# Performance work log

Measured on AMD Instinct MI355X. Metric: run time of the kernel, lower is better.

The kernel has to match this reference:

```python
import jax, jax.numpy as jnp
import numpy as np

N_NODES = 100000
N_EDGES = 3200000
N_GRAPHS = 512
IN_DIM = 128
H1, H2 = 32, 64
OUT_DIM = 1
LN_EPS = 1e-5


def setup_inputs() -> dict:
    key = jax.random.key(0)
    ks = jax.random.split(key, 12)
    x = jax.random.normal(ks[0], (N_NODES, IN_DIM), dtype=jnp.float32)
    edge_index = jax.random.randint(ks[1], (2, N_EDGES), 0, N_NODES, dtype=jnp.int64)
    batch = jnp.sort(jax.random.randint(ks[2], (N_NODES,), 0, N_GRAPHS, dtype=jnp.int64))
    def lin(k, fi, fo):
        s = 1.0 / np.sqrt(fi)
        return jax.random.uniform(k, (fi, fo), minval=-s, maxval=s, dtype=jnp.float32)
    params = {
        'W1': lin(ks[3], IN_DIM, H1), 'b1': jnp.zeros((H1,), jnp.float32),
        'g1': jnp.ones((H1,), jnp.float32), 'be1': jnp.zeros((H1,), jnp.float32),
        'W2': lin(ks[4], H1, H2), 'b2': jnp.zeros((H2,), jnp.float32),
        'g2': jnp.ones((H2,), jnp.float32), 'be2': jnp.zeros((H2,), jnp.float32),
        'Wc1': lin(ks[5], H2, 32), 'bc1': jnp.zeros((32,), jnp.float32),
        'Wc2': lin(ks[6], 32, OUT_DIM), 'bc2': jnp.zeros((OUT_DIM,), jnp.float32),
    }
    return {'x': x, 'edge_index': edge_index, 'batch': batch, **params}


def _gcn_norm(edge_index, n):
    # add self loops (PyG GCNConv default)
    loop = jnp.arange(n, dtype=edge_index.dtype)
    src = jnp.concatenate([edge_index[0], loop])
    dst = jnp.concatenate([edge_index[1], loop])
    deg = jax.ops.segment_sum(jnp.ones_like(dst, dtype=jnp.float32), dst, num_segments=n)
    dinv = jnp.where(deg > 0, 1.0 / jnp.sqrt(deg), 0.0)
    norm = dinv[src] * dinv[dst]  # [E+N]
    return src, dst, norm


def _gcn_conv(x, src, dst, norm, W, b, n):
    h = x @ W                                    # tiny GEMM
    msg = h[src] * norm[:, None]                 # gather + scale (memory-bound)
    agg = jax.ops.segment_sum(msg, dst, num_segments=n)  # scatter-add
    return agg + b


def _layernorm(x, g, b):
    mu = jnp.mean(x, axis=-1, keepdims=True)
    var = jnp.mean(jnp.square(x - mu), axis=-1, keepdims=True)
    return (x - mu) * jax.lax.rsqrt(var + LN_EPS) * g + b


def reference(x, edge_index, batch, W1, b1, g1, be1, W2, b2, g2, be2, Wc1, bc1, Wc2, bc2):
    n = x.shape[0]
    src, dst, norm = _gcn_norm(edge_index, n)
    # layer 1: GCNConv -> LayerNorm -> ReLU (dropout = identity in eval)
    h = jax.nn.relu(_layernorm(_gcn_conv(x, src, dst, norm, W1, b1, n), g1, be1))
    # layer 2
    h = jax.nn.relu(_layernorm(_gcn_conv(h, src, dst, norm, W2, b2, n), g2, be2))
    # global mean pool over graphs
    sums = jax.ops.segment_sum(h, batch, num_segments=N_GRAPHS)
    cnts = jax.ops.segment_sum(jnp.ones((n,), h.dtype), batch, num_segments=N_GRAPHS)
    pooled = sums / jnp.maximum(cnts, 1.0)[:, None]  # [G, H2]
    # classifier MLP
    z = jax.nn.relu(pooled @ Wc1 + bc1)
    return z @ Wc2 + bc2
```

## Files before the change

### kernel.cpp

```cpp
#include <hip/hip_runtime.h>
#include <hip/hip_fp16.h>

#define CAP 10240

__global__ __launch_bounds__(1024) void k_fused1(const int* __restrict__ ei,
                                                 const float* __restrict__ x,
                                                 const float* __restrict__ W1,
                                                 const int* __restrict__ batch,
                                                 int* __restrict__ gcnt,
                                                 int* __restrict__ bucketed,
                                                 __half* __restrict__ hs,
                                                 int* __restrict__ gstart,
                                                 int nA, int nG1, int NB,
                                                 int n, int E, int G) {
    __shared__ __align__(16) char smem[40960];
    int tid = threadIdx.x;
    int bid = blockIdx.x;
    if (bid < nA) {
        int* hist = (int*)smem;
        int* excl = hist + 512;
        int* gb   = excl + 512;
        int* ebuf = gb + 512;
        const int* src = ei;
        const int* dst = ei + E;
        for (int i = tid; i < 512; i += 1024) hist[i] = 0;
        __syncthreads();
        int e0 = bid * 8192;
        int d[8], sR[8];
#pragma unroll
        for (int k = 0; k < 8; k++) {
            int e = e0 + k * 1024 + tid;
            bool v = e < E;
            d[k]  = v ? dst[e] : -1;
            sR[k] = v ? src[e] : 0;
            if (v) atomicAdd(&hist[d[k] >> 8], 1);
        }
        __syncthreads();
        if (tid < 512) excl[tid] = hist[tid];
        __syncthreads();
        for (int off = 1; off < 512; off <<= 1) {
            int v2 = 0;
            if (tid < 512) v2 = excl[tid] + ((tid >= off) ? excl[tid - off] : 0);
            __syncthreads();
            if (tid < 512) excl[tid] = v2;
            __syncthreads();
        }
        if (tid < 512) {
            int c = hist[tid];
            int ex = excl[tid] - c;
            excl[tid] = ex;
            gb[tid] = c ? atomicAdd(&gcnt[tid], c) : 0;
            hist[tid] = ex;
        }
        __syncthreads();
#pragma unroll
        for (int k = 0; k < 8; k++) {
            if (d[k] >= 0) {
                int b = d[k] >> 8;
                int p = atomicAdd(&hist[b], 1);
                ebuf[p] = (sR[k] << 8) | (d[k] & 255);
            }
        }
        __syncthreads();
        if (tid < 512) {
            int lds0 = excl[tid];
            int cnt  = hist[tid] - lds0;
            int gb0  = gb[tid];
            int* dstp = bucketed + (size_t)tid * CAP;
            for (int k = 0; k < cnt; k++) {
                int gp = gb0 + k;
                if (gp < CAP) dstp[gp] = ebuf[lds0 + k];
            }
        }
    } else if (bid < nA + nG1) {
        float* Ws = (float*)smem;
        const float4* W4 = (const float4*)W1;
        ((float4*)Ws)[tid] = W4[tid];
        __syncthreads();
        int gb2 = bid - nA;
        int row = gb2 * 128 + (tid >> 3);
        int g8 = tid & 7;
        if (row >= n) return;
        const float4* x4 = (const float4*)x;
        const float4* Ws4 = (const float4*)Ws;
        float a0 = 0.f, a1 = 0.f, a2 = 0.f, a3 = 0.f;
#pragma unroll 4
        for (int j = 0; j < 32; j++) {
            float4 xq = x4[(size_t)row * 32 + j];
#pragma unroll
            for (int t = 0; t < 4; t++) {
                float xv = (t == 0) ? xq.x : (t == 1) ? xq.y : (t == 2) ? xq.z : xq.w;
                float4 wv = Ws4[(4 * j + t) * 8 + g8];
                a0 += xv * wv.x; a1 += xv * wv.y; a2 += xv * wv.z; a3 += xv * wv.w;
            }
        }
        __half2 o[2] = { __floats2half2_rn(a0, a1), __floats2half2_rn(a2, a3) };
        *(float2*)(hs + (size_t)row * 32 + g8 * 4) = *(const float2*)o;
    } else {
        int i = (bid - nA - nG1) * 1024 + tid;
        if (i > n) return;
        if (i == 0) {
            for (int g = 0; g <= batch[0]; g++) gstart[g] = 0;
        } else if (i == n) {
            for (int g = batch[n - 1] + 1; g <= G; g++) gstart[g] = n;
        } else {
            int b = batch[i], p = batch[i - 1];
            for (int g = p + 1; g <= b; g++) gstart[g] = i;
        }
    }
}

__global__ __launch_bounds__(512) void k_bucketB(const int* __restrict__ bucketed,
                                                 const int* __restrict__ gcnt,
                                                 int* __restrict__ csr,
                                                 int* __restrict__ offs,
                                                 int* __restrict__ deg,
                                                 float* __restrict__ dinv,
                                                 __half* __restrict__ hs, int n) {
    __shared__ int hist[256], scan_a[256], scan_b[256];
    __shared__ float sdinv[256];
    int b = blockIdx.x;
    int tid = threadIdx.x;
    int cnt = min(gcnt[b], CAP);
    int base = b * CAP;
    const int* ent = bucketed + (size_t)b * CAP;
    if (tid < 256) hist[tid] = 0;
    __syncthreads();
    for (int i = tid; i < cnt; i += 512) atomicAdd(&hist[ent[i] & 255], 1);
    __syncthreads();
    int h = (tid < 256) ? hist[tid] : 0;
    if (tid < 256) scan_a[tid] = h;
    __syncthreads();
    int* cur = scan_a;
    int* nxt = scan_b;
    for (int off = 1; off < 256; off <<= 1) {
        if (tid < 256) nxt[tid] = cur[tid] + ((tid >= off) ? cur[tid - off] : 0);
        __syncthreads();
        int* tmp = cur; cur = nxt; nxt = tmp;
    }
    if (tid < 256) {
        int ex = cur[tid] - h;
        float dv = rsqrtf((float)(h + 1));
        sdinv[tid] = dv;
        int node = b * 256 + tid;
        if (node < n) {
            offs[node] = base + ex;
            deg[node] = h;
            dinv[node] = dv;
        }
        hist[tid] = ex;
    }
    __syncthreads();
    for (int i = tid; i < cnt; i += 512) {
        int v = ent[i];
        int p = atomicAdd(&hist[v & 255], 1);
        csr[base + p] = v >> 8;
    }
    float4* hsv = (float4*)hs;
#pragma unroll
    for (int p = 0; p < 2; p++) {
        int idx = p * 512 + tid;
        int nl = idx >> 2, cg = idx & 3;
        int node = b * 256 + nl;
        if (node < n) {
            float dv = sdinv[nl];
            float4 raw = hsv[(size_t)node * 4 + cg];
            __half2* h2 = (__half2*)&raw;
            __half2 o[4];
#pragma unroll
            for (int j = 0; j < 4; j++) {
                float2 f = __half22float2(h2[j]);
                o[j] = __floats2half2_rn(f.x * dv, f.y * dv);
            }
            hsv[(size_t)node * 4 + cg] = *(const float4*)o;
        }
    }
}

template <bool DO_LN>
__global__ __launch_bounds__(256) void k_gather(const __half* __restrict__ hs,
                                                const int* __restrict__ csr,
                                                const int* __restrict__ offs,
                                                const int* __restrict__ deg,
                                                const float* __restrict__ dinv,
                                                const float* __restrict__ b,
                                                const float* __restrict__ g,
                                                const float* __restrict__ be,
                                                __half* __restrict__ out, int n) {
    int wave = threadIdx.x >> 6;
    int lane = threadIdx.x & 63;
    int q   = lane >> 4;
    int l16 = lane & 15;
    int nb  = l16 >> 2;
    int cg  = l16 & 3;
    int row = blockIdx.x * 16 + wave * 4 + q;
    if (row >= n) return;
    int base = offs[row];
    int dg = deg[row];
    const float4* hsv = (const float4*)hs;
    const float4 fz = make_float4(0.f, 0.f, 0.f, 0.f);
    const __half2 hz = __floats2half2_rn(0.f, 0.f);
    __half2 ha0[4], ha1[4];
#pragma unroll
    for (int j = 0; j < 4; j++) { ha0[j] = hz; ha1[j] = hz; }

    int e = nb;
    float4 r0 = (e     < dg) ? hsv[(size_t)csr[base + e    ] * 4 + cg] : fz;
    float4 r1 = (e + 4 < dg) ? hsv[(size_t)csr[base + e + 4] * 4 + cg] : fz;
    while (e < dg) {
        float4 p0 = (e +  8 < dg) ? hsv[(size_t)csr[base + e +  8] * 4 + cg] : fz;
        float4 p1 = (e + 12 < dg) ? hsv[(size_t)csr[base + e + 12] * 4 + cg] : fz;
        const __half2* h0 = (const __half2*)&r0;
        const __half2* h1 = (const __half2*)&r1;
#pragma unroll
        for (int j = 0; j < 4; j++) {
            ha0[j] = __hadd2(ha0[j], h0[j]);
            ha1[j] = __hadd2(ha1[j], h1[j]);
        }
        r0 = p0; r1 = p1; e += 8;
    }
    float acc[8];
#pragma unroll
    for (int j = 0; j < 4; j++) {
        float2 f0 = __half22float2(ha0[j]);
        float2 f1 = __half22float2(ha1[j]);
        acc[2 * j]     = f0.x + f1.x;
        acc[2 * j + 1] = f0.y + f1.y;
    }
#pragma unroll
    for (int m = 4; m <= 8; m <<= 1)
#pragma unroll
        for (int j = 0; j < 8; j++) acc[j] += __shfl_xor(acc[j], m, 64);
    float dv = dinv[row];
    float4 sraw = hsv[(size_t)row * 4 + cg];
    const __half2* sh2 = (const __half2*)&sraw;
    float a[8];
#pragma unroll
    for (int j = 0; j < 4; j++) {
        float2 f = __half22float2(sh2[j]);
        a[2 * j]     = (acc[2 * j]     + f.x) * dv;
        a[2 * j + 1] = (acc[2 * j + 1] + f.y) * dv;
    }
    if (DO_LN) {
        int c0 = cg * 8;
        float s = 0.f;
#pragma unroll
        for (int j = 0; j < 8; j++) { a[j] += b[c0 + j]; s += a[j]; }
#pragma unroll
        for (int m = 1; m <= 2; m <<= 1) s += __shfl_xor(s, m, 64);
        float mu = s * (1.0f / 32.0f);
        float v2 = 0.f;
#pragma unroll
        for (int j = 0; j < 8; j++) { a[j] -= mu; v2 += a[j] * a[j]; }
#pragma unroll
        for (int m = 1; m <= 2; m <<= 1) v2 += __shfl_xor(v2, m, 64);
        float inv = rsqrtf(v2 * (1.0f / 32.0f) + 1e-5f);
#pragma unroll
        for (int j = 0; j < 8; j++)
            a[j] = fmaxf(a[j] * inv * g[c0 + j] + be[c0 + j], 0.f) * dv;
    }
    if (nb == 0) {
        __half2 o[4];
#pragma unroll
        for (int j = 0; j < 4; j++) o[j] = __floats2half2_rn(a[2 * j], a[2 * j + 1]);
        ((float4*)out)[(size_t)row * 4 + cg] = *(const float4*)o;
    }
}

__global__ __launch_bounds__(512) void k_pool_cls(const __half* __restrict__ agg2,
                                                  const float* __restrict__ W2,
                                                  const float* __restrict__ b2,
                                                  const float* __restrict__ g2,
                                                  const float* __restrict__ be2,
                                                  const int* __restrict__ gstart,
                                                  const float* __restrict__ Wc1,
                                                  const float* __restrict__ bc1,
                                                  const float* __restrict__ Wc2,
                                                  const float* __restrict__ bc2,
                                                  float* __restrict__ out) {
    __shared__ float Ws[32 * 64];
    __shared__ float red[8 * 64];
    int tid = threadIdx.x;
    for (int i = tid; i < 32 * 64; i += 512) Ws[i] = W2[i];
    int g = blockIdx.x;
    int r0 = gstart[g], r1 = gstart[g + 1];
    int wave = tid >> 6, lane = tid & 63;
    float pacc = 0.0f;
    __syncthreads();
    for (int row = r0 + wave; row < r1; row += 8) {
        const float4* a4 = (const float4*)(agg2 + (size_t)row * 32);
        float4 r4[4];
#pragma unroll
        for (int q = 0; q < 4; q++) r4[q] = a4[q];
        const __half2* ah = (const __half2*)r4;
        float acc = b2[lane];
#pragma unroll
        for (int k2 = 0; k2 < 16; k2++) {
            float2 f = __half22float2(ah[k2]);
            acc += f.x * Ws[(2 * k2) * 64 + lane] + f.y * Ws[(2 * k2 + 1) * 64 + lane];
        }
        float s = acc;
#pragma unroll
        for (int m = 32; m >= 1; m >>= 1) s += __shfl_xor(s, m, 64);
        float mu = s * (1.0f / 64.0f);
        float d = acc - mu;
        float v = d * d;
#pragma unroll
        for (int m = 32; m >= 1; m >>= 1) v += __shfl_xor(v, m, 64);
        float val = d * rsqrtf(v * (1.0f / 64.0f) + 1e-5f) * g2[lane] + be2[lane];
        pacc += fmaxf(val, 0.0f);
    }
    red[wave * 64 + lane] = pacc;
    __syncthreads();
    if (wave == 0) {
        float p = 0.f;
#pragma unroll
        for (int w = 0; w < 8; w++) p += red[w * 64 + lane];
        p *= 1.0f / fmaxf((float)(r1 - r0), 1.0f);
        red[lane] = p;
    }
    __syncthreads();
    if (wave == 0 && lane < 32) {
        float zs = bc1[lane];
#pragma unroll
        for (int k = 0; k < 64; k++) zs += red[k] * Wc1[k * 32 + lane];
        float o = fmaxf(zs, 0.0f) * Wc2[lane];
#pragma unroll
        for (int m = 16; m >= 1; m >>= 1) o += __shfl_xor(o, m, 64);
        if (lane == 0) out[g] = o + bc2[0];
    }
}


extern "C" void kernel_launch(void* const* d_in, const int* in_sizes, int n_in,
                              void* d_out, int out_size, void* d_ws, size_t ws_size,
                              hipStream_t stream) {
    const float* x     = (const float*)d_in[0];
    const int*   ei    = (const int*)d_in[1];
    const int*   batch = (const int*)d_in[2];
    const float* W1  = (const float*)d_in[3];
    const float* b1  = (const float*)d_in[4];
    const float* g1  = (const float*)d_in[5];
    const float* be1 = (const float*)d_in[6];
    const float* W2  = (const float*)d_in[7];
    const float* b2  = (const float*)d_in[8];
    const float* g2  = (const float*)d_in[9];
    const float* be2 = (const float*)d_in[10];
    const float* Wc1 = (const float*)d_in[11];
    const float* bc1 = (const float*)d_in[12];
    const float* Wc2 = (const float*)d_in[13];
    const float* bc2 = (const float*)d_in[14];

    int n = in_sizes[0] / 128;
    int E = in_sizes[1] / 2;
    int G = out_size;
    int NB = (n + 255) >> 8;

    float* ws     = (float*)d_ws;
    float* dinv   = ws;
    int*   deg    = (int*)(dinv + n);
    int*   offs   = deg + n;
    int*   gcnt   = offs + n;
    int*   gstart = gcnt + 512;
    int*   csr    = gstart + 516;
    __half* hsA   = (__half*)(csr + (size_t)NB * CAP);
    int*   bucketed = (int*)(hsA + (size_t)n * 32);
    __half* hsB   = (__half*)bucketed;

    int nA  = (E + 8191) / 8192;
    int nG1 = (n + 127) / 128;
    int nGs = (n + 1024) / 1024;

    hipMemsetAsync(gcnt, 0, 512 * sizeof(int), stream);

    k_fused1<<<nA + nG1 + nGs, 1024, 0, stream>>>(ei, x, W1, batch, gcnt, bucketed,
                                                  hsA, gstart, nA, nG1, NB, n, E, G);
    k_bucketB<<<NB, 512, 0, stream>>>(bucketed, gcnt, csr, offs, deg, dinv, hsA, n);

    k_gather<true><<<(n + 15) / 16, 256, 0, stream>>>(hsA, csr, offs, deg, dinv,
                                                      b1, g1, be1, hsB, n);
    k_gather<false><<<(n + 15) / 16, 256, 0, stream>>>(hsB, csr, offs, deg, dinv,
                                                       nullptr, nullptr, nullptr, hsA, n);
    k_pool_cls<<<G, 512, 0, stream>>>(hsA, W2, b2, g2, be2, gstart,
                                      Wc1, bc1, Wc2, bc2, (float*)d_out);
}
```

Baseline: 215.1 us.

## Split feature columns into halves so each gather pass fits in cache

Stores the 32-wide half-precision node features as two 16-column planes and runs the neighbor gather separately on each plane. The intent is that each 3.2 MB plane stays resident in L2/MALL during random gathers. LayerNorm moves into a separate kernel, the final dinv scaling of layer 2 is folded into the pooling kernel, and the bucket copy-out is spread over 16 lanes per bucket. The cost is two extra gather launches plus one LN launch, re-reading the CSR indices for each half, and half-width rows per gather, which use fewer bytes per index fetched.

```diff
diff --git a/kernel.cpp b/kernel.cpp
--- a/kernel.cpp
+++ b/kernel.cpp
@@ -9,7 +9,8 @@
                                                  const int* __restrict__ batch,
                                                  int* __restrict__ gcnt,
                                                  int* __restrict__ bucketed,
-                                                 __half* __restrict__ hs,
+                                                 __half* __restrict__ hLo,
+                                                 __half* __restrict__ hHi,
                                                  int* __restrict__ gstart,
                                                  int nA, int nG1, int NB,
                                                  int n, int E, int G) {
@@ -62,15 +63,14 @@
             }
         }
         __syncthreads();
-        if (tid < 512) {
-            int lds0 = excl[tid];
-            int cnt  = hist[tid] - lds0;
-            int gb0  = gb[tid];
-            int* dstp = bucketed + (size_t)tid * CAP;
-            for (int k = 0; k < cnt; k++) {
-                int gp = gb0 + k;
-                if (gp < CAP) dstp[gp] = ebuf[lds0 + k];
-            }
+        int grp = tid >> 4, l = tid & 15;
+        for (int t = grp; t < 512; t += 64) {
+            int lds0 = excl[t];
+            int cnt  = hist[t] - lds0;
+            int gb0  = gb[t];
+            int* dstp = bucketed + (size_t)t * CAP + gb0;
+            for (int k = l; k < cnt; k += 16)
+                if (gb0 + k < CAP) dstp[k] = ebuf[lds0 + k];
         }
     } else if (bid < nA + nG1) {
         float* Ws = (float*)smem;
@@ -95,7 +95,9 @@
             }
         }
         __half2 o[2] = { __floats2half2_rn(a0, a1), __floats2half2_rn(a2, a3) };
-        *(float2*)(hs + (size_t)row * 32 + g8 * 4) = *(const float2*)o;
+        __half* dstp = (g8 < 4) ? (hLo + (size_t)row * 16 + g8 * 4)
+                                : (hHi + (size_t)row * 16 + (g8 - 4) * 4);
+        *(float2*)dstp = *(const float2*)o;
     } else {
         int i = (bid - nA - nG1) * 1024 + tid;
         if (i > n) return;
@@ -116,7 +118,8 @@
                                                  int* __restrict__ offs,
                                                  int* __restrict__ deg,
                                                  float* __restrict__ dinv,
-                                                 __half* __restrict__ hs, int n) {
+                                                 __half* __restrict__ hLo,
+                                                 __half* __restrict__ hHi, int n) {
     __shared__ int hist[256], scan_a[256], scan_b[256];
     __shared__ float sdinv[256];
     int b = blockIdx.x;
@@ -156,7 +159,8 @@
         int p = atomicAdd(&hist[v & 255], 1);
         csr[base + p] = v >> 8;
     }
-    float4* hsv = (float4*)hs;
+    float4* lo = (float4*)hLo;
+    float4* hi = (float4*)hHi;
 #pragma unroll
     for (int p = 0; p < 2; p++) {
         int idx = p * 512 + tid;
@@ -164,7 +168,9 @@
         int node = b * 256 + nl;
         if (node < n) {
             float dv = sdinv[nl];
-            float4 raw = hsv[(size_t)node * 4 + cg];
+            float4* ptr = (cg < 2) ? &lo[(size_t)node * 2 + cg]
+                                   : &hi[(size_t)node * 2 + (cg - 2)];
+            float4 raw = *ptr;
             __half2* h2 = (__half2*)&raw;
             __half2 o[4];
 #pragma unroll
@@ -172,28 +178,23 @@
                 float2 f = __half22float2(h2[j]);
                 o[j] = __floats2half2_rn(f.x * dv, f.y * dv);
             }
-            hsv[(size_t)node * 4 + cg] = *(const float4*)o;
-        }
-    }
-}
-
-template <bool DO_LN>
-__global__ __launch_bounds__(256) void k_gather(const __half* __restrict__ hs,
-                                                const int* __restrict__ csr,
-                                                const int* __restrict__ offs,
-                                                const int* __restrict__ deg,
-                                                const float* __restrict__ dinv,
-                                                const float* __restrict__ b,
-                                                const float* __restrict__ g,
-                                                const float* __restrict__ be,
-                                                __half* __restrict__ out, int n) {
+            *ptr = *(const float4*)o;
+        }
+    }
+}
+
+__global__ __launch_bounds__(256) void k_gather_h(const __half* __restrict__ hs,
+                                                  const int* __restrict__ csr,
+                                                  const int* __restrict__ offs,
+                                                  const int* __restrict__ deg,
+                                                  __half* __restrict__ out, int n) {
     int wave = threadIdx.x >> 6;
     int lane = threadIdx.x & 63;
-    int q   = lane >> 4;
-    int l16 = lane & 15;
-    int nb  = l16 >> 2;
-    int cg  = l16 & 3;
-    int row = blockIdx.x * 16 + wave * 4 + q;
+    int o  = lane >> 3;
+    int l8 = lane & 7;
+    int nb = l8 >> 1;
+    int cg = l8 & 1;
+    int row = blockIdx.x * 32 + wave * 8 + o;
     if (row >= n) return;
     int base = offs[row];
     int dg = deg[row];
@@ -205,11 +206,11 @@
     for (int j = 0; j < 4; j++) { ha0[j] = hz; ha1[j] = hz; }
 
     int e = nb;
-    float4 r0 = (e     < dg) ? hsv[(size_t)csr[base + e    ] * 4 + cg] : fz;
-    float4 r1 = (e + 4 < dg) ? hsv[(size_t)csr[base + e + 4] * 4 + cg] : fz;
+    float4 r0 = (e     < dg) ? hsv[(size_t)csr[base + e    ] * 2 + cg] : fz;
+    float4 r1 = (e + 4 < dg) ? hsv[(size_t)csr[base + e + 4] * 2 + cg] : fz;
     while (e < dg) {
-        float4 p0 = (e +  8 < dg) ? hsv[(size_t)csr[base + e +  8] * 4 + cg] : fz;
-        float4 p1 = (e + 12 < dg) ? hsv[(size_t)csr[base + e + 12] * 4 + cg] : fz;
+        float4 p0 = (e +  8 < dg) ? hsv[(size_t)csr[base + e +  8] * 2 + cg] : fz;
+        float4 p1 = (e + 12 < dg) ? hsv[(size_t)csr[base + e + 12] * 2 + cg] : fz;
         const __half2* h0 = (const __half2*)&r0;
         const __half2* h1 = (const __half2*)&r1;
 #pragma unroll
@@ -228,46 +229,74 @@
         acc[2 * j + 1] = f0.y + f1.y;
     }
 #pragma unroll
-    for (int m = 4; m <= 8; m <<= 1)
+    for (int m = 2; m <= 4; m <<= 1)
 #pragma unroll
         for (int j = 0; j < 8; j++) acc[j] += __shfl_xor(acc[j], m, 64);
+    float4 sraw = hsv[(size_t)row * 2 + cg];
+    const __half2* sh2 = (const __half2*)&sraw;
+    if (nb == 0) {
+        __half2 ov[4];
+#pragma unroll
+        for (int j = 0; j < 4; j++) {
+            float2 f = __half22float2(sh2[j]);
+            ov[j] = __floats2half2_rn(acc[2 * j] + f.x, acc[2 * j + 1] + f.y);
+        }
+        ((float4*)out)[(size_t)row * 2 + cg] = *(const float4*)ov;
+    }
+}
+
+__global__ __launch_bounds__(256) void k_ln_split(const __half* __restrict__ aggLo,
+                                                  const __half* __restrict__ aggHi,
+                                                  const float* __restrict__ dinv,
+                                                  const float* __restrict__ b,
+                                                  const float* __restrict__ g,
+                                                  const float* __restrict__ be,
+                                                  __half* __restrict__ outLo,
+                                                  __half* __restrict__ outHi, int n) {
+    int tid = threadIdx.x;
+    int rl = tid >> 2;
+    int l4 = tid & 3;
+    int row = blockIdx.x * 64 + rl;
+    if (row >= n) return;
+    const float4* lo = (const float4*)aggLo;
+    const float4* hi = (const float4*)aggHi;
+    float4 raw = (l4 < 2) ? lo[(size_t)row * 2 + l4] : hi[(size_t)row * 2 + (l4 - 2)];
     float dv = dinv[row];
-    float4 sraw = hsv[(size_t)row * 4 + cg];
-    const __half2* sh2 = (const __half2*)&sraw;
+    int c0 = l4 * 8;
+    const __half2* h2 = (const __half2*)&raw;
     float a[8];
+    float s = 0.f;
 #pragma unroll
     for (int j = 0; j < 4; j++) {
-        float2 f = __half22float2(sh2[j]);
-        a[2 * j]     = (acc[2 * j]     + f.x) * dv;
-        a[2 * j + 1] = (acc[2 * j + 1] + f.y) * dv;
-    }
-    if (DO_LN) {
-        int c0 = cg * 8;
-        float s = 0.f;
-#pragma unroll
-        for (int j = 0; j < 8; j++) { a[j] += b[c0 + j]; s += a[j]; }
-#pragma unroll
-        for (int m = 1; m <= 2; m <<= 1) s += __shfl_xor(s, m, 64);
-        float mu = s * (1.0f / 32.0f);
-        float v2 = 0.f;
-#pragma unroll
-        for (int j = 0; j < 8; j++) { a[j] -= mu; v2 += a[j] * a[j]; }
-#pragma unroll
-        for (int m = 1; m <= 2; m <<= 1) v2 += __shfl_xor(v2, m, 64);
-        float inv = rsqrtf(v2 * (1.0f / 32.0f) + 1e-5f);
-#pragma unroll
-        for (int j = 0; j < 8; j++)
-            a[j] = fmaxf(a[j] * inv * g[c0 + j] + be[c0 + j], 0.f) * dv;
-    }
-    if (nb == 0) {
-        __half2 o[4];
-#pragma unroll
-        for (int j = 0; j < 4; j++) o[j] = __floats2half2_rn(a[2 * j], a[2 * j + 1]);
-        ((float4*)out)[(size_t)row * 4 + cg] = *(const float4*)o;
-    }
-}
-
-__global__ __launch_bounds__(512) void k_pool_cls(const __half* __restrict__ agg2,
+        float2 f = __half22float2(h2[j]);
+        a[2 * j]     = f.x * dv + b[c0 + 2 * j];
+        a[2 * j + 1] = f.y * dv + b[c0 + 2 * j + 1];
+        s += a[2 * j] + a[2 * j + 1];
+    }
+#pragma unroll
+    for (int m = 1; m <= 2; m <<= 1) s += __shfl_xor(s, m, 64);
+    float mu = s * (1.0f / 32.0f);
+    float v2 = 0.f;
+#pragma unroll
+    for (int j = 0; j < 8; j++) { a[j] -= mu; v2 += a[j] * a[j]; }
+#pragma unroll
+    for (int m = 1; m <= 2; m <<= 1) v2 += __shfl_xor(v2, m, 64);
+    float inv = rsqrtf(v2 * (1.0f / 32.0f) + 1e-5f);
+    __half2 ov[4];
+#pragma unroll
+    for (int j = 0; j < 4; j++) {
+        float y0 = fmaxf(a[2 * j]     * inv * g[c0 + 2 * j]     + be[c0 + 2 * j],     0.f) * dv;
+        float y1 = fmaxf(a[2 * j + 1] * inv * g[c0 + 2 * j + 1] + be[c0 + 2 * j + 1], 0.f) * dv;
+        ov[j] = __floats2half2_rn(y0, y1);
+    }
+    float4* dstp = (l4 < 2) ? ((float4*)outLo + (size_t)row * 2 + l4)
+                            : ((float4*)outHi + (size_t)row * 2 + (l4 - 2));
+    *dstp = *(const float4*)ov;
+}
+
+__global__ __launch_bounds__(512) void k_pool_cls(const __half* __restrict__ aggLo,
+                                                  const __half* __restrict__ aggHi,
+                                                  const float* __restrict__ dinv,
                                                   const float* __restrict__ W2,
                                                   const float* __restrict__ b2,
                                                   const float* __restrict__ g2,
@@ -287,18 +316,23 @@
     int wave = tid >> 6, lane = tid & 63;
     float pacc = 0.0f;
     __syncthreads();
+    const float4* lo = (const float4*)aggLo;
+    const float4* hi = (const float4*)aggHi;
     for (int row = r0 + wave; row < r1; row += 8) {
-        const float4* a4 = (const float4*)(agg2 + (size_t)row * 32);
         float4 r4[4];
-#pragma unroll
-        for (int q = 0; q < 4; q++) r4[q] = a4[q];
+        r4[0] = lo[(size_t)row * 2];
+        r4[1] = lo[(size_t)row * 2 + 1];
+        r4[2] = hi[(size_t)row * 2];
+        r4[3] = hi[(size_t)row * 2 + 1];
+        float dv = dinv[row];
         const __half2* ah = (const __half2*)r4;
-        float acc = b2[lane];
+        float dot = 0.f;
 #pragma unroll
         for (int k2 = 0; k2 < 16; k2++) {
             float2 f = __half22float2(ah[k2]);
-            acc += f.x * Ws[(2 * k2) * 64 + lane] + f.y * Ws[(2 * k2 + 1) * 64 + lane];
-        }
+            dot += f.x * Ws[(2 * k2) * 64 + lane] + f.y * Ws[(2 * k2 + 1) * 64 + lane];
+        }
+        float acc = b2[lane] + dv * dot;
         float s = acc;
 #pragma unroll
         for (int m = 32; m >= 1; m >>= 1) s += __shfl_xor(s, m, 64);
@@ -363,9 +397,11 @@
     int*   gcnt   = offs + n;
     int*   gstart = gcnt + 512;
     int*   csr    = gstart + 516;
-    __half* hsA   = (__half*)(csr + (size_t)NB * CAP);
-    int*   bucketed = (int*)(hsA + (size_t)n * 32);
-    __half* hsB   = (__half*)bucketed;
+    __half* h0Lo  = (__half*)(csr + (size_t)NB * CAP);
+    __half* h0Hi  = h0Lo + (size_t)n * 16;
+    int*   bucketed = (int*)(h0Hi + (size_t)n * 16);
+    __half* h1Lo  = (__half*)bucketed;
+    __half* h1Hi  = h1Lo + (size_t)n * 16;
 
     int nA  = (E + 8191) / 8192;
     int nG1 = (n + 127) / 128;
@@ -374,13 +410,17 @@
     hipMemsetAsync(gcnt, 0, 512 * sizeof(int), stream);
 
     k_fused1<<<nA + nG1 + nGs, 1024, 0, stream>>>(ei, x, W1, batch, gcnt, bucketed,
-                                                  hsA, gstart, nA, nG1, NB, n, E, G);
-    k_bucketB<<<NB, 512, 0, stream>>>(bucketed, gcnt, csr, offs, deg, dinv, hsA, n);
-
-    k_gather<true><<<(n + 15) / 16, 256, 0, stream>>>(hsA, csr, offs, deg, dinv,
-                                                      b1, g1, be1, hsB, n);
-    k_gather<false><<<(n + 15) / 16, 256, 0, stream>>>(hsB, csr, offs, deg, dinv,
-                                                       nullptr, nullptr, nullptr, hsA, n);
-    k_pool_cls<<<G, 512, 0, stream>>>(hsA, W2, b2, g2, be2, gstart,
+                                                  h0Lo, h0Hi, gstart, nA, nG1, NB, n, E, G);
+    k_bucketB<<<NB, 512, 0, stream>>>(bucketed, gcnt, csr, offs, deg, dinv,
+                                      h0Lo, h0Hi, n);
+
+    k_gather_h<<<(n + 31) / 32, 256, 0, stream>>>(h0Lo, csr, offs, deg, h1Lo, n);
+    k_gather_h<<<(n + 31) / 32, 256, 0, stream>>>(h0Hi, csr, offs, deg, h1Hi, n);
+    k_ln_split<<<(n + 63) / 64, 256, 0, stream>>>(h1Lo, h1Hi, dinv, b1, g1, be1,
+                                                  h0Lo, h0Hi, n);
+    k_gather_h<<<(n + 31) / 32, 256, 0, stream>>>(h0Lo, csr, offs, deg, h1Lo, n);
+    k_gather_h<<<(n + 31) / 32, 256, 0, stream>>>(h0Hi, csr, offs, deg, h1Hi, n);
+
+    k_pool_cls<<<G, 512, 0, stream>>>(h1Lo, h1Hi, dinv, W2, b2, g2, be2, gstart,
                                       Wc1, bc1, Wc2, bc2, (float*)d_out);
 }
```

Measured after the change: 235.2 us. +9.3%, slower.
